# Performance work log

Hardware: AMD Instinct MI355X
Metric: run time of the kernel (lower is better)

Reference implementation:

```python
import jax, jax.numpy as jnp
import numpy as np

NH = 4
MAX_BUF = 1024
EPS = 1e-5


def _ln(x, w, b):
    mu = jnp.mean(x, axis=-1, keepdims=True)
    var = jnp.var(x, axis=-1, keepdims=True)
    return (x - mu) * jax.lax.rsqrt(var + EPS) * w + b


def _mha(xq, xkv, w_qkv, b_qkv, w_o, b_o, key_mask=None):
    D = xq.shape[-1]
    dh = D // NH
    q = xq @ w_qkv[:D].T + b_qkv[:D]
    k = xkv @ w_qkv[D:2 * D].T + b_qkv[D:2 * D]
    v = xkv @ w_qkv[2 * D:].T + b_qkv[2 * D:]
    sp = lambda t: t.reshape(t.shape[0], t.shape[1], NH, dh).transpose(0, 2, 1, 3)
    q, k, v = sp(q), sp(k), sp(v)
    s = jnp.einsum('bhqd,bhkd->bhqk', q, k) / jnp.sqrt(jnp.asarray(dh, q.dtype))
    if key_mask is not None:
        s = jnp.where(key_mask[:, None, None, :], -1e9, s)
    a = jax.nn.softmax(s, axis=-1)
    o = jnp.einsum('bhqk,bhkd->bhqd', a, v)
    o = o.transpose(0, 2, 1, 3).reshape(o.shape[0], o.shape[2], D)
    return o @ w_o.T + b_o


def _conv1d(x, w, b):  # x: (B,C,T), w: (O,I,K) k=3 pad=1
    y = jax.lax.conv_general_dilated(x, w, (1,), [(1, 1)], dimension_numbers=('NCH', 'OIH', 'NCH'))
    return y + b[None, :, None]


def _vpred(xt, c1w, c1b, l1w, l1b, c2w, c2b, l2w, l2b, lw, lb):
    # Faithful to the torch module: LayerNorm(256)/Linear(256,1) act on the LAST
    # axis of the (B,256,T) conv output, which requires T == 256.
    h = _ln(jax.nn.relu(_conv1d(xt, c1w, c1b)), l1w, l1b)
    h = _ln(jax.nn.relu(_conv1d(h, c2w, c2b)), l2w, l2b)
    return (h @ lw.T + lb)[..., 0]  # (B, 256)


def _length_regulate(x, duration, lengths):
    # x: (B,T,D), duration: (B,T) float. Faithful parallel version of the
    # sequential scatter: tokens that are padded, have dur<=0, or would
    # overflow max_len are skipped (pos does not advance).
    B, T, D = x.shape
    durs = jnp.round(duration).astype(jnp.int32)
    max_len = jnp.clip(jnp.round(jnp.sum(duration, axis=1)).max().astype(jnp.int32), 0, MAX_BUF)
    valid_t = jnp.arange(T)[None, :] < lengths[:, None]

    def per_seq(dur_b, val_b):
        def step(pos, dv):
            d, v = dv
            ok = v & (d > 0) & (pos + d <= max_len)
            de = jnp.where(ok, d, 0)
            return pos + de, de
        return jax.lax.scan(step, jnp.asarray(0, jnp.int32), (dur_b, val_b))[1]

    dur_eff = jax.vmap(per_seq)(durs, valid_t)          # (B,T)
    ends = jnp.cumsum(dur_eff, axis=1)                  # token t fills [ends[t-1], ends[t])
    frames = jnp.arange(MAX_BUF)
    tok = jax.vmap(lambda e: jnp.searchsorted(e, frames, side='right'))(ends)  # (B,MAX_BUF)
    in_range = frames[None, :] < ends[:, -1:]
    g = jnp.take_along_axis(x, jnp.clip(tok, 0, T - 1)[..., None], axis=1)
    return jnp.where(in_range[..., None], g, jnp.zeros((), x.dtype))


def _forward(te, lengths, enc_qkv_w, enc_qkv_b, enc_out_w, enc_out_b, enc_ln1_w, enc_ln1_b, enc_ff1_w, enc_ff1_b, enc_ff2_w, enc_ff2_b, enc_ln2_w, enc_ln2_b, vp_c1_w, vp_c1_b, vp_l1_w, vp_l1_b, vp_c2_w, vp_c2_b, vp_l2_w, vp_l2_b, vp_lin_w, vp_lin_b, dec_sa_qkv_w, dec_sa_qkv_b, dec_sa_out_w, dec_sa_out_b, dec_ca_qkv_w, dec_ca_qkv_b, dec_ca_out_w, dec_ca_out_b, dec_ln1_w, dec_ln1_b, dec_ln2_w, dec_ln2_b, dec_ln3_w, dec_ln3_b, dec_ff1_w, dec_ff1_b, dec_ff2_w, dec_ff2_b, mel_w, mel_b):
    B, T, D = te.shape
    mask = jnp.arange(T)[None, :] >= lengths[:, None]  # src_key_padding_mask
    x = te
    for i in range(enc_qkv_w.shape[0]):  # post-norm TransformerEncoderLayer, gelu
        sa = _mha(x, x, enc_qkv_w[i], enc_qkv_b[i], enc_out_w[i], enc_out_b[i], mask)
        x = _ln(x + sa, enc_ln1_w[i], enc_ln1_b[i])
        ff = jax.nn.gelu(x @ enc_ff1_w[i].T + enc_ff1_b[i], approximate=False) @ enc_ff2_w[i].T + enc_ff2_b[i]
        x = _ln(x + ff, enc_ln2_w[i], enc_ln2_b[i])
    enc = x
    xt = enc.transpose(0, 2, 1)  # (B, D, T)
    duration, pitch, energy = [
        _vpred(xt, vp_c1_w[j], vp_c1_b[j], vp_l1_w[j], vp_l1_b[j], vp_c2_w[j], vp_c2_b[j], vp_l2_w[j], vp_l2_b[j], vp_lin_w[j], vp_lin_b[j])
        for j in range(3)]
    y = _length_regulate(enc, duration, lengths)  # (B, MAX_BUF, D)
    for i in range(dec_sa_qkv_w.shape[0]):  # post-norm TransformerDecoderLayer
        sa = _mha(y, y, dec_sa_qkv_w[i], dec_sa_qkv_b[i], dec_sa_out_w[i], dec_sa_out_b[i])
        y = _ln(y + sa, dec_ln1_w[i], dec_ln1_b[i])
        ca = _mha(y, enc, dec_ca_qkv_w[i], dec_ca_qkv_b[i], dec_ca_out_w[i], dec_ca_out_b[i])
        y = _ln(y + ca, dec_ln2_w[i], dec_ln2_b[i])
        ff = jax.nn.gelu(y @ dec_ff1_w[i].T + dec_ff1_b[i], approximate=False) @ dec_ff2_w[i].T + dec_ff2_b[i]
        y = _ln(y + ff, dec_ln3_w[i], dec_ln3_b[i])
    mel = (y @ mel_w.T + mel_b).transpose(0, 2, 1)  # (B, n_mel, MAX_BUF)
    return mel, duration, pitch, energy


def setup_inputs() -> dict:
    B, T, D, FF, NM, L = 32, 256, 256, 1024, 80, 4
    ks = iter(jax.random.split(jax.random.key(0), 80))

    def w(scale, *shape):
        return (scale * jax.random.normal(next(ks), shape)).astype(jnp.float32)

    z = lambda *s: jnp.zeros(s, jnp.float32)
    o = lambda *s: jnp.ones(s, jnp.float32)
    inp = {}
    inp['text_embeddings'] = jax.random.normal(next(ks), (B, T, D), jnp.float32)
    inp['text_lengths'] = jax.random.randint(next(ks), (B,), 64, T + 1, dtype=jnp.int32)
    inp.update(
        enc_qkv_w=w(0.02, L, 3 * D, D), enc_qkv_b=z(L, 3 * D), enc_out_w=w(0.02, L, D, D), enc_out_b=z(L, D),
        enc_ln1_w=o(L, D), enc_ln1_b=z(L, D), enc_ff1_w=w(0.02, L, FF, D), enc_ff1_b=z(L, FF),
        enc_ff2_w=w(0.02, L, D, FF), enc_ff2_b=z(L, D), enc_ln2_w=o(L, D), enc_ln2_b=z(L, D),
        vp_c1_w=w(0.05, 3, 256, D, 3), vp_c1_b=z(3, 256), vp_l1_w=o(3, 256), vp_l1_b=z(3, 256),
        vp_c2_w=w(0.05, 3, 256, 256, 3), vp_c2_b=z(3, 256), vp_l2_w=o(3, 256), vp_l2_b=z(3, 256),
        vp_lin_w=w(0.1, 3, 1, 256), vp_lin_b=jnp.array([[4.0], [0.0], [0.0]], jnp.float32),
        dec_sa_qkv_w=w(0.02, L, 3 * D, D), dec_sa_qkv_b=z(L, 3 * D), dec_sa_out_w=w(0.02, L, D, D), dec_sa_out_b=z(L, D),
        dec_ca_qkv_w=w(0.02, L, 3 * D, D), dec_ca_qkv_b=z(L, 3 * D), dec_ca_out_w=w(0.02, L, D, D), dec_ca_out_b=z(L, D),
        dec_ln1_w=o(L, D), dec_ln1_b=z(L, D), dec_ln2_w=o(L, D), dec_ln2_b=z(L, D), dec_ln3_w=o(L, D), dec_ln3_b=z(L, D),
        dec_ff1_w=w(0.02, L, FF, D), dec_ff1_b=z(L, FF), dec_ff2_w=w(0.02, L, D, FF), dec_ff2_b=z(L, D),
        mel_w=w(0.02, NM, D), mel_b=z(NM))
    return inp


def reference(text_embeddings, text_lengths, enc_qkv_w, enc_qkv_b, enc_out_w, enc_out_b, enc_ln1_w, enc_ln1_b, enc_ff1_w, enc_ff1_b, enc_ff2_w, enc_ff2_b, enc_ln2_w, enc_ln2_b, vp_c1_w, vp_c1_b, vp_l1_w, vp_l1_b, vp_c2_w, vp_c2_b, vp_l2_w, vp_l2_b, vp_lin_w, vp_lin_b, dec_sa_qkv_w, dec_sa_qkv_b, dec_sa_out_w, dec_sa_out_b, dec_ca_qkv_w, dec_ca_qkv_b, dec_ca_out_w, dec_ca_out_b, dec_ln1_w, dec_ln1_b, dec_ln2_w, dec_ln2_b, dec_ln3_w, dec_ln3_b, dec_ff1_w, dec_ff1_b, dec_ff2_w, dec_ff2_b, mel_w, mel_b):
    return _forward(text_embeddings, text_lengths, enc_qkv_w, enc_qkv_b, enc_out_w, enc_out_b, enc_ln1_w, enc_ln1_b, enc_ff1_w, enc_ff1_b, enc_ff2_w, enc_ff2_b, enc_ln2_w, enc_ln2_b, vp_c1_w, vp_c1_b, vp_l1_w, vp_l1_b, vp_c2_w, vp_c2_b, vp_l2_w, vp_l2_b, vp_lin_w, vp_lin_b, dec_sa_qkv_w, dec_sa_qkv_b, dec_sa_out_w, dec_sa_out_b, dec_ca_qkv_w, dec_ca_qkv_b, dec_ca_out_w, dec_ca_out_b, dec_ln1_w, dec_ln1_b, dec_ln2_w, dec_ln2_b, dec_ln3_w, dec_ln3_b, dec_ff1_w, dec_ff1_b, dec_ff2_w, dec_ff2_b, mel_w, mel_b)
```

## Files before the change

### kernel.cpp

```cpp
#include <hip/hip_runtime.h>
#include <hip/hip_bf16.h>
#include <cstdint>
#include <cstddef>


#define B_ 32
#define T_ 256
#define D_ 256
#define NH_ 4
#define FF_ 1024
#define MAXBUF_ 1024
#define NMEL_ 80

typedef __attribute__((ext_vector_type(8))) short short8;
typedef __attribute__((ext_vector_type(4))) float f32x4;

__device__ __forceinline__ unsigned short f2bf(float x) {
  unsigned int u = __float_as_uint(x);
  return (unsigned short)((u + 0x7fffu + ((u >> 16) & 1u)) >> 16);
}
__device__ __forceinline__ float bf2f(unsigned short h) {
  return __uint_as_float(((unsigned int)h) << 16);
}

#define GLD16(g, s)                                                         \
  __builtin_amdgcn_global_load_lds(                                         \
      (__attribute__((address_space(1))) void*)(g),                         \
      (__attribute__((address_space(3))) void*)(s), 16, 0, 0)

__global__ __launch_bounds__(256) void gemm_k(
    const float* __restrict__ A, const float* __restrict__ W,
    const float* __restrict__ bias, float* __restrict__ C,
    int M, int N, int K, int epi)
{
  __shared__ float As[16][64];
  __shared__ float Ws[16][64];
  const int tid = threadIdx.x;
  const int tx = tid & 15, ty = tid >> 4;
  const int bm = blockIdx.x * 64, bn = blockIdx.y * 64;
  const int lm = tid & 63, lk = tid >> 6;
  float acc[4][4] = {{0.f,0.f,0.f,0.f},{0.f,0.f,0.f,0.f},{0.f,0.f,0.f,0.f},{0.f,0.f,0.f,0.f}};
  const bool aok = (bm + lm) < M;
  const bool wok = (bn + lm) < N;
  const float* Ap = A + (size_t)(bm + lm) * K + lk * 4;
  const float* Wp = W + (size_t)(bn + lm) * K + lk * 4;
  for (int k0 = 0; k0 < K; k0 += 16) {
    float4 av = make_float4(0.f, 0.f, 0.f, 0.f);
    float4 wv = make_float4(0.f, 0.f, 0.f, 0.f);
    if (aok) av = *(const float4*)(Ap + k0);
    if (wok) wv = *(const float4*)(Wp + k0);
    As[lk*4+0][lm] = av.x; As[lk*4+1][lm] = av.y; As[lk*4+2][lm] = av.z; As[lk*4+3][lm] = av.w;
    Ws[lk*4+0][lm] = wv.x; Ws[lk*4+1][lm] = wv.y; Ws[lk*4+2][lm] = wv.z; Ws[lk*4+3][lm] = wv.w;
    __syncthreads();
#pragma unroll
    for (int kk = 0; kk < 16; ++kk) {
      float4 a4 = *(const float4*)&As[kk][ty * 4];
      float4 b4 = *(const float4*)&Ws[kk][tx * 4];
      float aa[4] = {a4.x, a4.y, a4.z, a4.w};
      float bb[4] = {b4.x, b4.y, b4.z, b4.w};
#pragma unroll
      for (int i = 0; i < 4; ++i)
#pragma unroll
        for (int j = 0; j < 4; ++j)
          acc[i][j] += aa[i] * bb[j];
    }
    __syncthreads();
  }
#pragma unroll
  for (int i = 0; i < 4; ++i) {
    int gm = bm + ty * 4 + i;
    if (gm >= M) continue;
#pragma unroll
    for (int j = 0; j < 4; ++j) {
      int gn = bn + tx * 4 + j;
      if (gn >= N) continue;
      float v = acc[i][j] + bias[gn];
      if (epi == 1) v = 0.5f * v * (1.0f + erff(v * 0.70710678118654752f));
      C[(size_t)gm * N + gn] = v;
    }
  }
}

__global__ __launch_bounds__(256, 2) void gemm2_k(
    const float* __restrict__ A, const float* __restrict__ W,
    const float* __restrict__ bias, float* __restrict__ C,
    int M, int N, int K, int epi)
{
  __shared__ float As[16][128];
  __shared__ float Bs[16][128];
  const int tid = threadIdx.x;
  const int tx = tid & 15, ty = tid >> 4;
  const int bm = blockIdx.x * 128, bn = blockIdx.y * 128;
  const int r = tid & 127, ks = (tid >> 7) * 8;
  f32x4 acc[8][2];
#pragma unroll
  for (int i = 0; i < 8; ++i) {
    acc[i][0] = (f32x4){0.f, 0.f, 0.f, 0.f};
    acc[i][1] = (f32x4){0.f, 0.f, 0.f, 0.f};
  }
  const float* Ap = A + (size_t)(bm + r) * K + ks;
  const float* Wp = W + (size_t)(bn + r) * K + ks;
  for (int k0 = 0; k0 < K; k0 += 16) {
    float4 a0 = *(const float4*)(Ap + k0);
    float4 a1 = *(const float4*)(Ap + k0 + 4);
    float4 w0 = *(const float4*)(Wp + k0);
    float4 w1 = *(const float4*)(Wp + k0 + 4);
    __syncthreads();
    As[ks+0][r] = a0.x; As[ks+1][r] = a0.y; As[ks+2][r] = a0.z; As[ks+3][r] = a0.w;
    As[ks+4][r] = a1.x; As[ks+5][r] = a1.y; As[ks+6][r] = a1.z; As[ks+7][r] = a1.w;
    Bs[ks+0][r] = w0.x; Bs[ks+1][r] = w0.y; Bs[ks+2][r] = w0.z; Bs[ks+3][r] = w0.w;
    Bs[ks+4][r] = w1.x; Bs[ks+5][r] = w1.y; Bs[ks+6][r] = w1.z; Bs[ks+7][r] = w1.w;
    __syncthreads();
#pragma unroll
    for (int kk = 0; kk < 16; ++kk) {
      f32x4 bA = *(const f32x4*)&Bs[kk][tx * 4];
      f32x4 bB = *(const f32x4*)&Bs[kk][tx * 4 + 64];
      float4 aA = *(const float4*)&As[kk][ty * 4];
      float4 aB = *(const float4*)&As[kk][ty * 4 + 64];
      float av[8] = {aA.x, aA.y, aA.z, aA.w, aB.x, aB.y, aB.z, aB.w};
#pragma unroll
      for (int i = 0; i < 8; ++i) {
        acc[i][0] += bA * av[i];
        acc[i][1] += bB * av[i];
      }
    }
  }
#pragma unroll
  for (int i = 0; i < 8; ++i) {
    int gm = bm + (i >> 2) * 64 + ty * 4 + (i & 3);
#pragma unroll
    for (int half = 0; half < 2; ++half) {
      int gn = bn + half * 64 + tx * 4;
      float4 o;
      o.x = acc[i][half][0] + bias[gn + 0];
      o.y = acc[i][half][1] + bias[gn + 1];
      o.z = acc[i][half][2] + bias[gn + 2];
      o.w = acc[i][half][3] + bias[gn + 3];
      if (epi == 1) {
        o.x = 0.5f * o.x * (1.0f + erff(o.x * 0.70710678118654752f));
        o.y = 0.5f * o.y * (1.0f + erff(o.y * 0.70710678118654752f));
        o.z = 0.5f * o.z * (1.0f + erff(o.z * 0.70710678118654752f));
        o.w = 0.5f * o.w * (1.0f + erff(o.w * 0.70710678118654752f));
      }
      *(float4*)(C + (size_t)gm * N + gn) = o;
    }
  }
}

__global__ __launch_bounds__(256, 2) void gemm2p_k(
    const float* __restrict__ A, const float* __restrict__ W,
    float* __restrict__ Dst, float* __restrict__ Palt,
    int M, int N, int kChunk, int Ktot)
{
  __shared__ float As[16][128];
  __shared__ float Bs[16][128];
  const int tid = threadIdx.x;
  const int tx = tid & 15, ty = tid >> 4;
  const int bm = blockIdx.x * 128, bn = blockIdx.y * 128;
  const int z = blockIdx.z;
  const int r = tid & 127, ks = (tid >> 7) * 8;
  f32x4 acc[8][2];
#pragma unroll
  for (int i = 0; i < 8; ++i) {
    acc[i][0] = (f32x4){0.f, 0.f, 0.f, 0.f};
    acc[i][1] = (f32x4){0.f, 0.f, 0.f, 0.f};
// ... 22 lines not shown
      for (int i = 0; i < 8; ++i) {
        acc[i][0] += bA * av[i];
        acc[i][1] += bB * av[i];
      }
    }
  }
  float* Out = (z == 0) ? Dst : (Palt + (size_t)(z - 1) * ((size_t)M * N));
#pragma unroll
  for (int i = 0; i < 8; ++i) {
    int gm = bm + (i >> 2) * 64 + ty * 4 + (i & 3);
#pragma unroll
    for (int half = 0; half < 2; ++half) {
      int gn = bn + half * 64 + tx * 4;
      float4 o;
      o.x = acc[i][half][0]; o.y = acc[i][half][1];
      o.z = acc[i][half][2]; o.w = acc[i][half][3];
      *(float4*)(Out + (size_t)gm * N + gn) = o;
    }
  }
}

__global__ __launch_bounds__(256) void rsum_k(
    float* __restrict__ C, const float* __restrict__ Palt,
    const float* __restrict__ bias, int Sm1, int N, size_t MN, int epi)
{
  size_t i = ((size_t)blockIdx.x * 256 + threadIdx.x) * 4;
  if (i >= MN) return;
  float4 a = *(const float4*)(C + i);
  for (int s = 0; s < Sm1; ++s) {
    float4 b = *(const float4*)(Palt + (size_t)s * MN + i);
    a.x += b.x; a.y += b.y; a.z += b.z; a.w += b.w;
  }
  int col = (int)(i % (size_t)N);
  a.x += bias[col + 0]; a.y += bias[col + 1];
  a.z += bias[col + 2]; a.w += bias[col + 3];
  if (epi == 1) {
    a.x = 0.5f * a.x * (1.0f + erff(a.x * 0.70710678118654752f));
    a.y = 0.5f * a.y * (1.0f + erff(a.y * 0.70710678118654752f));
    a.z = 0.5f * a.z * (1.0f + erff(a.z * 0.70710678118654752f));
    a.w = 0.5f * a.w * (1.0f + erff(a.w * 0.70710678118654752f));
  }
  *(float4*)(C + i) = a;
}

__global__ __launch_bounds__(256) void attn_k(
    const float* __restrict__ Qp, int qStride,
    const float* __restrict__ Kp, int kStride,
    const float* __restrict__ Vp, int vStride,
    float* __restrict__ Op, int Tq, int Tkv,
    const int* __restrict__ lengths)
{
  const int b = blockIdx.z, h = blockIdx.y, qt = blockIdx.x;
  const int tid = threadIdx.x;
  const int tx = tid & 15, ty = tid >> 4;
  const int lr = tid & 63, lq = tid >> 6;

  __shared__ float Qs[64][64];
  __shared__ float KT[64][64];
  __shared__ float Sm[64][65];

  {
    const float* q = Qp + (size_t)(b * Tq + qt * 64 + lr) * qStride + h * 64 + lq * 16;
    float4 v0 = ((const float4*)q)[0];
    float4 v1 = ((const float4*)q)[1];
    float4 v2 = ((const float4*)q)[2];
    float4 v3 = ((const float4*)q)[3];
    *(float4*)&Qs[lr][lq*16 + 0]  = v0;
    *(float4*)&Qs[lr][lq*16 + 4]  = v1;
    *(float4*)&Qs[lr][lq*16 + 8]  = v2;
    *(float4*)&Qs[lr][lq*16 + 12] = v3;
  }

  float m_reg[4], l_reg[4], o[4][4];
#pragma unroll
  for (int i = 0; i < 4; ++i) {
    m_reg[i] = -INFINITY; l_reg[i] = 0.f;
#pragma unroll
    for (int j = 0; j < 4; ++j) o[i][j] = 0.f;
  }

  const int len_b = lengths ? lengths[b] : 0x7fffffff;
  const int nkt = Tkv >> 6;

  for (int kt = 0; kt < nkt; ++kt) {
    __syncthreads();
    {
      const float* kp = Kp + (size_t)(b * Tkv + kt * 64 + lr) * kStride + h * 64 + lq * 16;
      float4 v[4];
      v[0] = ((const float4*)kp)[0]; v[1] = ((const float4*)kp)[1];
      v[2] = ((const float4*)kp)[2]; v[3] = ((const float4*)kp)[3];
#pragma unroll
      for (int u = 0; u < 4; ++u) {
        KT[lq*16 + u*4 + 0][lr] = v[u].x;
        KT[lq*16 + u*4 + 1][lr] = v[u].y;
        KT[lq*16 + u*4 + 2][lr] = v[u].z;
        KT[lq*16 + u*4 + 3][lr] = v[u].w;
      }
    }
    __syncthreads();

    float s[4][4] = {{0.f,0.f,0.f,0.f},{0.f,0.f,0.f,0.f},{0.f,0.f,0.f,0.f},{0.f,0.f,0.f,0.f}};
#pragma unroll
    for (int d4 = 0; d4 < 16; ++d4) {
      float4 qv[4], kv[4];
#pragma unroll
      for (int i = 0; i < 4; ++i) qv[i] = *(const float4*)&Qs[ty*4 + i][d4*4];
#pragma unroll
      for (int dd = 0; dd < 4; ++dd) kv[dd] = *(const float4*)&KT[d4*4 + dd][tx*4];
#pragma unroll
      for (int i = 0; i < 4; ++i) {
        s[i][0] += qv[i].x*kv[0].x + qv[i].y*kv[1].x + qv[i].z*kv[2].x + qv[i].w*kv[3].x;
        s[i][1] += qv[i].x*kv[0].y + qv[i].y*kv[1].y + qv[i].z*kv[2].y + qv[i].w*kv[3].y;
        s[i][2] += qv[i].x*kv[0].z + qv[i].y*kv[1].z + qv[i].z*kv[2].z + qv[i].w*kv[3].z;
        s[i][3] += qv[i].x*kv[0].w + qv[i].y*kv[1].w + qv[i].z*kv[2].w + qv[i].w*kv[3].w;
      }
    }

    float alpha[4];
#pragma unroll
    for (int i = 0; i < 4; ++i) {
      float pm = -INFINITY;
#pragma unroll
      for (int j = 0; j < 4; ++j) {
        int kg = kt * 64 + tx * 4 + j;
        float v = s[i][j] * 0.125f;
        if (kg >= len_b) v = -1e9f;
        s[i][j] = v;
        pm = fmaxf(pm, v);
      }
#pragma unroll
      for (int off = 1; off < 16; off <<= 1) pm = fmaxf(pm, __shfl_xor(pm, off));
      float mn = fmaxf(m_reg[i], pm);
      alpha[i] = expf(m_reg[i] - mn);
      float ls = 0.f;
#pragma unroll
      for (int j = 0; j < 4; ++j) {
        float p = expf(s[i][j] - mn);
        Sm[ty*4 + i][tx*4 + j] = p;
        ls += p;
      }
#pragma unroll
      for (int off = 1; off < 16; off <<= 1) ls += __shfl_xor(ls, off);
      l_reg[i] = l_reg[i] * alpha[i] + ls;
      m_reg[i] = mn;
    }
    __syncthreads();

    {
      const float* vp = Vp + (size_t)(b * Tkv + kt * 64 + lr) * vStride + h * 64 + lq * 16;
      float4 v0 = ((const float4*)vp)[0];
      float4 v1 = ((const float4*)vp)[1];
      float4 v2 = ((const float4*)vp)[2];
      float4 v3 = ((const float4*)vp)[3];
      *(float4*)&KT[lr][lq*16 + 0]  = v0;
      *(float4*)&KT[lr][lq*16 + 4]  = v1;
      *(float4*)&KT[lr][lq*16 + 8]  = v2;
      *(float4*)&KT[lr][lq*16 + 12] = v3;
    }
    __syncthreads();

#pragma unroll
    for (int i = 0; i < 4; ++i) {
      o[i][0] *= alpha[i]; o[i][1] *= alpha[i]; o[i][2] *= alpha[i]; o[i][3] *= alpha[i];
    }
#pragma unroll 8
    for (int c = 0; c < 64; ++c) {
      float4 vv = *(const float4*)&KT[c][tx * 4];
#pragma unroll
      for (int i = 0; i < 4; ++i) {
        float p = Sm[ty*4 + i][c];
        o[i][0] += p * vv.x; o[i][1] += p * vv.y; o[i][2] += p * vv.z; o[i][3] += p * vv.w;
      }
    }
  }

#pragma unroll
  for (int i = 0; i < 4; ++i) {
    float inv = 1.f / l_reg[i];
    float4 r;
    r.x = o[i][0] * inv; r.y = o[i][1] * inv; r.z = o[i][2] * inv; r.w = o[i][3] * inv;
    *(float4*)(Op + (size_t)(b * Tq + qt * 64 + ty * 4 + i) * 256 + h * 64 + tx * 4) = r;
  }
}

__global__ __launch_bounds__(256) void gemm_bf_k(
    const unsigned short* __restrict__ A, const unsigned short* __restrict__ W,
    const float* __restrict__ bias, unsigned short* __restrict__ C,
    int M, int N, int K, int epi)
{
  __shared__ __align__(16) short As[128 * 32];
  __shared__ __align__(16) short Bs[128 * 32];
  const int tid = threadIdx.x;
  const int lane = tid & 63, w = tid >> 6;
  const int g = lane >> 4, li = lane & 15;
  const int wr = (w >> 1) * 64, wc = (w & 1) * 64;
  const int bm = blockIdx.x * 128, bn = blockIdx.y * 128;

  f32x4 acc[4][4];
#pragma unroll
  for (int m = 0; m < 4; ++m)
#pragma unroll
    for (int n = 0; n < 4; ++n)
      acc[m][n] = (f32x4){0.f, 0.f, 0.f, 0.f};

  const int srow = tid >> 2, scol = (tid & 3) * 8;
  const unsigned short* Ag = A + (size_t)(bm + srow) * K + scol;
  const unsigned short* Wg = W + (size_t)(bn + srow) * K + scol;

  for (int k0 = 0; k0 < K; k0 += 32) {
    __syncthreads();
    GLD16(Ag + k0, &As[tid * 8]);
    GLD16(Ag + k0 + (size_t)64 * K, &As[tid * 8 + 2048]);
    GLD16(Wg + k0, &Bs[tid * 8]);
    GLD16(Wg + k0 + (size_t)64 * K, &Bs[tid * 8 + 2048]);
    __syncthreads();
    short8 af[4], bf[4];
#pragma unroll
    for (int m = 0; m < 4; ++m) af[m] = *(const short8*)&As[(wr + m * 16 + li) * 32 + g * 8];
#pragma unroll
    for (int n = 0; n < 4; ++n) bf[n] = *(const short8*)&Bs[(wc + n * 16 + li) * 32 + g * 8];
#pragma unroll
    for (int m = 0; m < 4; ++m)
#pragma unroll
      for (int n = 0; n < 4; ++n)
        acc[m][n] = __builtin_amdgcn_mfma_f32_16x16x32_bf16(af[m], bf[n], acc[m][n], 0, 0, 0);
  }

#pragma unroll
  for (int m = 0; m < 4; ++m) {
#pragma unroll
    for (int n = 0; n < 4; ++n) {
      int col = bn + wc + n * 16 + li;
      float bv = bias[col];
#pragma unroll
      for (int r = 0; r < 4; ++r) {
        int row = bm + wr + m * 16 + g * 4 + r;
        float v = acc[m][n][r] + bv;
        if (epi == 1) v = 0.5f * v * (1.0f + erff(v * 0.70710678118654752f));
        C[(size_t)row * N + col] = f2bf(v);
      }
// ... 144 lines not shown
          float p = __expf(s[m][n][r] - mn);
          ls += p;
          int col = n * 16 + li;
          Ps[row * 64 + (col ^ ((row & 7) << 3))] = (short)f2bf(p);
        }
#pragma unroll
        for (int off = 1; off < 16; off <<= 1) ls += __shfl_xor(ls, off);
        l_reg[m][r] = l_reg[m][r] * alpha[m][r] + ls;
        m_reg[m][r] = mn;
      }

#pragma unroll
    for (int m = 0; m < 2; ++m) {
      f32x4 al = (f32x4){alpha[m][0], alpha[m][1], alpha[m][2], alpha[m][3]};
#pragma unroll
      for (int n = 0; n < 4; ++n) o[m][n] *= al;
    }
    short8 ap[2][2];
#pragma unroll
    for (int m = 0; m < 2; ++m)
#pragma unroll
      for (int ks = 0; ks < 2; ++ks) {
        int row = w * 32 + m * 16 + li;
        ap[m][ks] = *(const short8*)&Ps[row * 64 + (((ks * 4 + g) ^ (row & 7)) << 3)];
      }
    __builtin_amdgcn_s_setprio(1);
#pragma unroll
    for (int m = 0; m < 2; ++m)
#pragma unroll
      for (int n = 0; n < 4; ++n)
#pragma unroll
        for (int ks = 0; ks < 2; ++ks) {
          int d = n * 16 + li;
          short8 bv = *(const short8*)&VTs[d * 64 + (((ks * 4 + g) ^ (d & 7)) << 3)];
          o[m][n] = __builtin_amdgcn_mfma_f32_16x16x32_bf16(ap[m][ks], bv, o[m][n], 0, 0, 0);
        }
    __builtin_amdgcn_s_setprio(0);
  }

#pragma unroll
  for (int m = 0; m < 2; ++m)
#pragma unroll
    for (int n = 0; n < 4; ++n)
#pragma unroll
      for (int r = 0; r < 4; ++r) {
        float v = o[m][n][r] / l_reg[m][r];
        Op[(size_t)(b * Tq + qt * 128 + w * 32 + m * 16 + g * 4 + r) * 256 + h * 64 + n * 16 + li] = f2bf(v);
      }
}

__global__ __launch_bounds__(256) void addln_k(
    const float* __restrict__ X, const float* __restrict__ R,
    const float* __restrict__ w, const float* __restrict__ bias,
    float* __restrict__ Out, int rows)
{
  int tid = threadIdx.x, wv = tid >> 6, ln = tid & 63;
  int row = blockIdx.x * 4 + wv;
  if (row >= rows) return;
  const float* xp = X + (size_t)row * 256;
  float v[4];
#pragma unroll
  for (int u = 0; u < 4; ++u) v[u] = xp[u * 64 + ln];
  if (R) {
    const float* rp = R + (size_t)row * 256;
#pragma unroll
    for (int u = 0; u < 4; ++u) v[u] += rp[u * 64 + ln];
  }
  float s = v[0] + v[1] + v[2] + v[3];
#pragma unroll
  for (int off = 1; off < 64; off <<= 1) s += __shfl_xor(s, off);
  float mean = s * (1.f / 256.f);
  float c[4], sq = 0.f;
#pragma unroll
  for (int u = 0; u < 4; ++u) { c[u] = v[u] - mean; sq += c[u] * c[u]; }
#pragma unroll
  for (int off = 1; off < 64; off <<= 1) sq += __shfl_xor(sq, off);
  float rs = 1.f / sqrtf(sq * (1.f / 256.f) + 1e-5f);
  float* op = Out + (size_t)row * 256;
#pragma unroll
  for (int u = 0; u < 4; ++u)
    op[u * 64 + ln] = c[u] * rs * w[u * 64 + ln] + bias[u * 64 + ln];
}

__global__ __launch_bounds__(256) void addln2_k(
    const float* __restrict__ X, const unsigned short* __restrict__ Rbf,
    const float* __restrict__ w, const float* __restrict__ bias,
    float* __restrict__ Out, unsigned short* __restrict__ OutBf, int rows)
{
  int tid = threadIdx.x, wv = tid >> 6, ln = tid & 63;
  int row = blockIdx.x * 4 + wv;
  if (row >= rows) return;
  const float* xp = X + (size_t)row * 256;
  const unsigned short* rp = Rbf + (size_t)row * 256;
  float v[4];
#pragma unroll
  for (int u = 0; u < 4; ++u) v[u] = xp[u * 64 + ln] + bf2f(rp[u * 64 + ln]);
  float s = v[0] + v[1] + v[2] + v[3];
#pragma unroll
  for (int off = 1; off < 64; off <<= 1) s += __shfl_xor(s, off);
  float mean = s * (1.f / 256.f);
  float c[4], sq = 0.f;
#pragma unroll
  for (int u = 0; u < 4; ++u) { c[u] = v[u] - mean; sq += c[u] * c[u]; }
#pragma unroll
  for (int off = 1; off < 64; off <<= 1) sq += __shfl_xor(sq, off);
  float rs = 1.f / sqrtf(sq * (1.f / 256.f) + 1e-5f);
  float* op = Out + (size_t)row * 256;
  unsigned short* ob = OutBf + (size_t)row * 256;
#pragma unroll
  for (int u = 0; u < 4; ++u) {
    float y = c[u] * rs * w[u * 64 + ln] + bias[u * 64 + ln];
    op[u * 64 + ln] = y;
    ob[u * 64 + ln] = f2bf(y);
  }
}

__global__ void cvt_k(const float* __restrict__ in, unsigned short* __restrict__ out, int n)
{
  int i = (blockIdx.x * 256 + threadIdx.x) * 4;
  if (i >= n) return;
  float4 v = *(const float4*)(in + i);
  unsigned short o[4] = {f2bf(v.x), f2bf(v.y), f2bf(v.z), f2bf(v.w)};
  *(ushort4*)(out + i) = *(ushort4*)o;
}

__global__ __launch_bounds__(256) void conv_k(
    const float* __restrict__ X, const float* __restrict__ Wt,
    const float* __restrict__ bias, float* __restrict__ Yo, int relu)
{
  const int b = blockIdx.z;
  const int o0 = blockIdx.y * 64, t0 = blockIdx.x * 64;
  const int tid = threadIdx.x, tx = tid & 15, ty = tid >> 4;
  __shared__ __align__(16) float xs[16][68];
  __shared__ __align__(16) float ws_s[64][48];
  float acc[4][4] = {{0.f,0.f,0.f,0.f},{0.f,0.f,0.f,0.f},{0.f,0.f,0.f,0.f},{0.f,0.f,0.f,0.f}};
  for (int i0 = 0; i0 < 256; i0 += 16) {
    for (int idx = tid; idx < 16 * 68; idx += 256) {
      int ic = idx / 68, tt = idx - ic * 68;
      int t = t0 + tt - 1;
      xs[ic][tt] = (tt < 66 && t >= 0 && t < 256)
                       ? X[((size_t)b * 256 + (i0 + ic)) * 256 + t] : 0.f;
    }
    for (int f4 = tid; f4 < 768; f4 += 256) {
      int oo = f4 / 12, seg = f4 - oo * 12;
      float4 v = *(const float4*)(Wt + (size_t)(o0 + oo) * 768 + i0 * 3 + seg * 4);
      *(float4*)&ws_s[oo][seg * 4] = v;
    }
    __syncthreads();
#pragma unroll
    for (int ic = 0; ic < 16; ++ic) {
      float4 xa = *(const float4*)&xs[ic][tx * 4];
      float4 xb = *(const float4*)&xs[ic][tx * 4 + 4];
      float xr[6] = {xa.x, xa.y, xa.z, xa.w, xb.x, xb.y};
#pragma unroll
      for (int i = 0; i < 4; ++i) {
        const float* wr = &ws_s[ty * 4 + i][ic * 3];
        float w0 = wr[0], w1 = wr[1], w2 = wr[2];
#pragma unroll
        for (int j = 0; j < 4; ++j)
          acc[i][j] += w0 * xr[j] + w1 * xr[j + 1] + w2 * xr[j + 2];
      }
    }
    __syncthreads();
  }
#pragma unroll
  for (int i = 0; i < 4; ++i) {
    int oo = o0 + ty * 4 + i;
    float bv = bias[oo];
#pragma unroll
    for (int j = 0; j < 4; ++j) {
      float v = acc[i][j] + bv;
      if (relu) v = fmaxf(v, 0.f);
      Yo[((size_t)b * 256 + oo) * 256 + t0 + tx * 4 + j] = v;
    }
  }
}

__global__ void transp_k(const float* __restrict__ In, float* __restrict__ Out)
{
  int b = blockIdx.z, t0 = blockIdx.x * 32, d0 = blockIdx.y * 32;
  __shared__ float tile[32][33];
  int tx = threadIdx.x, ty = threadIdx.y;
#pragma unroll
  for (int q = 0; q < 4; ++q)
    tile[ty + q * 8][tx] = In[((size_t)b * 256 + t0 + ty + q * 8) * 256 + d0 + tx];
  __syncthreads();
#pragma unroll
  for (int q = 0; q < 4; ++q)
    Out[((size_t)b * 256 + d0 + ty + q * 8) * 256 + t0 + tx] = tile[tx][ty + q * 8];
}

__global__ __launch_bounds__(256) void rowdot_k(
    const float* __restrict__ H, const float* __restrict__ lw,
    const float* __restrict__ lb, float* __restrict__ of32,
    float* __restrict__ oout, int rows)
{
  int tid = threadIdx.x, wv = tid >> 6, ln = tid & 63;
  int row = blockIdx.x * 4 + wv;
  if (row >= rows) return;
  const float* hp = H + (size_t)row * 256;
  float s = 0.f;
#pragma unroll
  for (int u = 0; u < 4; ++u) s += hp[u * 64 + ln] * lw[u * 64 + ln];
#pragma unroll
  for (int off = 1; off < 64; off <<= 1) s += __shfl_xor(s, off);
  if (ln == 0) {
    float v = s + lb[0];
    of32[row] = v;
    oout[row] = v;
  }
}

__global__ void maxlen_k(const float* __restrict__ dur, int* __restrict__ ml)
{
  __shared__ float rnds[32];
  int tid = threadIdx.x, wv = tid >> 6, ln = tid & 63;
  for (int b = wv; b < 32; b += 4) {
    const float* dp = dur + (size_t)b * 256;
    float s = dp[ln] + dp[64 + ln] + dp[128 + ln] + dp[192 + ln];
#pragma unroll
    for (int off = 1; off < 64; off <<= 1) s += __shfl_xor(s, off);
    if (ln == 0) rnds[b] = rintf(s);
  }
  __syncthreads();
  if (tid == 0) {
    float m = rnds[0];
    for (int b = 1; b < 32; ++b) m = fmaxf(m, rnds[b]);
    int v = (int)m;
    v = v < 0 ? 0 : (v > MAXBUF_ ? MAXBUF_ : v);
    *ml = v;
  }
}

__global__ void reg_k(const float* __restrict__ dur, const int* __restrict__ lens,
                      const int* __restrict__ ml, int* __restrict__ tok)
{
  int b = blockIdx.x;
  __shared__ float sdur[256];
  __shared__ int ends[256];
  int tid = threadIdx.x;
  sdur[tid] = dur[(size_t)b * 256 + tid];
  __syncthreads();
  if (tid == 0) {
    int maxlen = *ml, len = lens[b], pos = 0;
    for (int t = 0; t < 256; ++t) {
      int d = (int)rintf(sdur[t]);
      bool ok = (t < len) && (d > 0) && (pos + d <= maxlen);
      if (ok) pos += d;
      ends[t] = pos;
    }
  }
  __syncthreads();
  int total = ends[255];
  for (int f = tid; f < MAXBUF_; f += 256) {
    int lo = 0, hi = 256;
    while (lo < hi) { int mid = (lo + hi) >> 1; if (ends[mid] <= f) lo = mid + 1; else hi = mid; }
    int tc = lo > 255 ? 255 : lo;
    tok[(size_t)b * MAXBUF_ + f] = (f < total) ? tc : -1;
  }
}

__global__ void gather_k(const float* __restrict__ enc, const int* __restrict__ tok,
                         float* __restrict__ Y)
{
  int rf = blockIdx.x;
  int b = rf >> 10;
  int t = tok[rf];
  float4* dst = (float4*)(Y + (size_t)rf * 256);
  int ln = threadIdx.x;
  if (t >= 0) {
    const float4* src = (const float4*)(enc + ((size_t)b * 256 + t) * 256);
    dst[ln] = src[ln];
  } else {
    dst[ln] = make_float4(0.f, 0.f, 0.f, 0.f);
  }
}

__global__ __launch_bounds__(256) void meltr_k(
    const float* __restrict__ MEL, float* __restrict__ out)
{
  int b = blockIdx.z, m0 = blockIdx.y * 16, f0 = blockIdx.x * 64;
  __shared__ float t[16][65];
  int tid = threadIdx.x;
  {
    int f_i = tid >> 4, m_i = tid & 15;
#pragma unroll
    for (int q = 0; q < 4; ++q)
      t[m_i][f_i + q * 16] = MEL[((size_t)b * 1024 + f0 + f_i + q * 16) * 80 + m0 + m_i];
  }
  __syncthreads();
  {
    int f = tid & 63, my = tid >> 6;
#pragma unroll
    for (int q = 0; q < 4; ++q) {
      int m = my * 4 + q;
      out[((size_t)b * NMEL_ + m0 + m) * MAXBUF_ + f0 + f] = t[m][f];
    }
  }
}

extern "C" void kernel_launch(void* const* d_in, const int* in_sizes, int n_in,
                              void* d_out, int out_size, void* d_ws, size_t ws_size,
                              hipStream_t stream)
{
  (void)in_sizes; (void)n_in; (void)out_size;

  const float* te   = (const float*)d_in[0];
  const int*   lens = (const int*)d_in[1];
  const float* e_qkv_w = (const float*)d_in[2];
  const float* e_qkv_b = (const float*)d_in[3];
  const float* e_out_w = (const float*)d_in[4];
  const float* e_out_b = (const float*)d_in[5];
  const float* e_ln1_w = (const float*)d_in[6];
  const float* e_ln1_b = (const float*)d_in[7];
  const float* e_ff1_w = (const float*)d_in[8];
  const float* e_ff1_b = (const float*)d_in[9];
  const float* e_ff2_w = (const float*)d_in[10];
  const float* e_ff2_b = (const float*)d_in[11];
  const float* e_ln2_w = (const float*)d_in[12];
  const float* e_ln2_b = (const float*)d_in[13];
  const float* c1w = (const float*)d_in[14];
  const float* c1b = (const float*)d_in[15];
  const float* l1w = (const float*)d_in[16];
  const float* l1b = (const float*)d_in[17];
  const float* c2w = (const float*)d_in[18];
  const float* c2b = (const float*)d_in[19];
  const float* l2w = (const float*)d_in[20];
  const float* l2b = (const float*)d_in[21];
  const float* linw = (const float*)d_in[22];
  const float* linb = (const float*)d_in[23];
  const float* d_sa_qkv_w = (const float*)d_in[24];
  const float* d_sa_qkv_b = (const float*)d_in[25];
  const float* d_sa_out_w = (const float*)d_in[26];
  const float* d_sa_out_b = (const float*)d_in[27];
  const float* d_ca_qkv_w = (const float*)d_in[28];
  const float* d_ca_qkv_b = (const float*)d_in[29];
  const float* d_ca_out_w = (const float*)d_in[30];
  const float* d_ca_out_b = (const float*)d_in[31];
  const float* d_ln1_w = (const float*)d_in[32];
  const float* d_ln1_b = (const float*)d_in[33];
  const float* d_ln2_w = (const float*)d_in[34];
  const float* d_ln2_b = (const float*)d_in[35];
  const float* d_ln3_w = (const float*)d_in[36];
  const float* d_ln3_b = (const float*)d_in[37];
  const float* d_ff1_w = (const float*)d_in[38];
  const float* d_ff1_b = (const float*)d_in[39];
  const float* d_ff2_w = (const float*)d_in[40];
  const float* d_ff2_b = (const float*)d_in[41];
  const float* melw = (const float*)d_in[42];
  const float* melb = (const float*)d_in[43];
  float* out = (float*)d_out;

  char* p = (char*)d_ws;
  float* Y   = (float*)p;            p += 8388608ull * 4;
  float* ENC = (float*)p;            p += 2097152ull * 4;
  unsigned short* ENCbf = (unsigned short*)p; p += 2097152ull * 2;
  unsigned short* Wsaqkv = (unsigned short*)p; p += 786432ull * 2;
  unsigned short* Wsaout = (unsigned short*)p; p += 262144ull * 2;
  unsigned short* Wcaqkv = (unsigned short*)p; p += 786432ull * 2;
  unsigned short* Wcaout = (unsigned short*)p; p += 262144ull * 2;
  unsigned short* Wff1   = (unsigned short*)p; p += 1048576ull * 2;
  unsigned short* Wff2   = (unsigned short*)p; p += 1048576ull * 2;
  float* DUR = (float*)p;            p += 24576ull * 4;
  int* TOK   = (int*)p;              p += 32768ull * 4;
  int* MAXL  = (int*)p;              p += 4096;
  size_t fixed_b = (size_t)(p - (char*)d_ws);

  int grp = 1;
  {
    const int cand[6] = {32, 16, 8, 4, 2, 1};
    for (int c = 0; c < 6; ++c) {
      if (fixed_b + (size_t)cand[c] * 1835008ull * 2 <= ws_size) { grp = cand[c]; break; }
    }
  }
  unsigned short* REG = (unsigned short*)p;
  unsigned short* Ybf   = REG;
  unsigned short* ADDbf = REG + (size_t)grp * 262144;
  unsigned short* AObf  = REG + (size_t)grp * 524288;
  unsigned short* UN    = REG + (size_t)grp * 786432;
  unsigned short* VTb   = REG + (size_t)grp * 1572864;
  int grp_e = grp * 2 > 32 ? 32 : grp * 2;
  float* P0e = (float*)REG;
  float* P1e = P0e + (size_t)grp_e * 262144;
  float* P2e = P1e + (size_t)grp_e * 65536;
  float* ENCT = Y;
  float* H1   = Y + 2097152;
  float* H2   = Y + 4194304;
  float* MEL  = ENC;

  auto gemm = [&](const float* A, const float* W, const float* bias, float* C,
                  int M, int N, int K, int epi) {
    dim3 g((M + 63) / 64, (N + 63) / 64);
    gemm_k<<<g, dim3(256), 0, stream>>>(A, W, bias, C, M, N, K, epi);
  };
  auto gemm2 = [&](const float* A, const float* W, const float* bias, float* C,
                   int M, int N, int K, int epi) {
    dim3 g(M / 128, N / 128);
    gemm2_k<<<g, dim3(256), 0, stream>>>(A, W, bias, C, M, N, K, epi);
  };
  auto gemm2s = [&](const float* A, const float* W, const float* bias, float* C,
                    int M, int N, int K, int S, int epi) {
    int kChunk = K / S;
    gemm2p_k<<<dim3(M / 128, N / 128, S), dim3(256), 0, stream>>>(
        A, W, C, Y, M, N, kChunk, K);
    size_t MN = (size_t)M * N;
    rsum_k<<<dim3((unsigned)(MN / 1024)), dim3(256), 0, stream>>>(
        C, Y, bias, S - 1, N, MN, epi);
  };
  auto gemm_bf = [&](const unsigned short* A, const unsigned short* W, const float* bias,
                     unsigned short* C, int M, int N, int K, int epi) {
    dim3 g(M / 128, N / 128);
    gemm_bf_k<<<g, dim3(256), 0, stream>>>(A, W, bias, C, M, N, K, epi);
  };
  auto addln = [&](const float* X, const float* R, const float* w, const float* b,
                   float* O, int rows) {
    addln_k<<<dim3((rows + 3) / 4), dim3(256), 0, stream>>>(X, R, w, b, O, rows);
  };
  auto addln2 = [&](const float* X, const unsigned short* Rbf, const float* w, const float* b,
                    float* O, unsigned short* Obf, int rows) {
    addln2_k<<<dim3((rows + 3) / 4), dim3(256), 0, stream>>>(X, Rbf, w, b, O, Obf, rows);
  };
  auto cvt = [&](const float* in, unsigned short* o, int n) {
    cvt_k<<<dim3(n / 1024), dim3(256), 0, stream>>>(in, o, n);
  };

  cvt(d_sa_qkv_w, Wsaqkv, 786432);
  cvt(d_sa_out_w, Wsaout, 262144);
  cvt(d_ca_qkv_w, Wcaqkv, 786432);
  cvt(d_ca_out_w, Wcaout, 262144);
  cvt(d_ff1_w, Wff1, 1048576);
  cvt(d_ff2_w, Wff2, 1048576);

  for (int i = 0; i < 4; ++i) {
    for (int g0 = 0; g0 < B_; g0 += grp_e) {
      int rows = grp_e * T_;
      const size_t off = (size_t)g0 * T_ * D_;
      const float* xin = (i == 0) ? te + off : ENC + off;
      gemm2s(xin, e_qkv_w + (size_t)i * 196608, e_qkv_b + i * 768, P0e, rows, 768, 256, 2, 0);
      attn_k<<<dim3(T_ / 64, NH_, grp_e), dim3(256), 0, stream>>>(
          P0e, 768, P0e + 256, 768, P0e + 512, 768, P1e, T_, T_, lens + g0);
      gemm2s(P1e, e_out_w + (size_t)i * 65536, e_out_b + i * 256, P2e, rows, 256, 256, 4, 0);
      addln(xin, P2e, e_ln1_w + i * 256, e_ln1_b + i * 256, ENC + off, rows);
      gemm2s(ENC + off, e_ff1_w + (size_t)i * 262144, e_ff1_b + i * 1024, P0e, rows, 1024, 256, 2, 1);
      gemm2s(P0e, e_ff2_w + (size_t)i * 262144, e_ff2_b + i * 256, P2e, rows, 256, 1024, 4, 0);
      addln(ENC + off, P2e, e_ln2_w + i * 256, e_ln2_b + i * 256, ENC + off, rows);
    }
  }
  cvt(ENC, ENCbf, 2097152);

  transp_k<<<dim3(8, 8, B_), dim3(32, 8), 0, stream>>>(ENC, ENCT);
  for (int j = 0; j < 3; ++j) {
    conv_k<<<dim3(4, 4, B_), dim3(256), 0, stream>>>(
        ENCT, c1w + (size_t)j * 196608, c1b + j * 256, H1, 1);
    addln(H1, nullptr, l1w + j * 256, l1b + j * 256, H1, B_ * T_);
    conv_k<<<dim3(4, 4, B_), dim3(256), 0, stream>>>(
        H1, c2w + (size_t)j * 196608, c2b + j * 256, H2, 1);
    addln(H2, nullptr, l2w + j * 256, l2b + j * 256, H2, B_ * T_);
    rowdot_k<<<dim3(B_ * T_ / 4), dim3(256), 0, stream>>>(
        H2, linw + j * 256, linb + j, DUR + (size_t)j * 8192,
        out + 2621440 + (size_t)j * 8192, B_ * T_);
  }

  maxlen_k<<<dim3(1), dim3(256), 0, stream>>>(DUR, MAXL);
  reg_k<<<dim3(B_), dim3(256), 0, stream>>>(DUR, lens, MAXL, TOK);
  gather_k<<<dim3(B_ * MAXBUF_), dim3(64), 0, stream>>>(ENC, TOK, Y);

  for (int i = 0; i < 4; ++i) {
    for (int g0 = 0; g0 < B_; g0 += grp) {
      int rows = grp * MAXBUF_;
      float* Yg = Y + (size_t)g0 * MAXBUF_ * D_;
      if (i == 0 || grp != B_)
        cvt(Yg, Ybf, rows * 256);
      gemm_bf(Ybf, Wsaqkv + (size_t)i * 196608, d_sa_qkv_b + i * 768, UN, rows, 768, 256, 0);
      trv_k<<<dim3(MAXBUF_ / 64, NH_, grp), dim3(256), 0, stream>>>(UN + 512, 768, VTb, MAXBUF_);
      attn_bf_k<<<dim3(MAXBUF_ / 128, NH_, grp), dim3(256), 0, stream>>>(
          UN, 768, UN + 256, 768, VTb, AObf, MAXBUF_, MAXBUF_);
      gemm_bf(AObf, Wsaout + (size_t)i * 65536, d_sa_out_b + i * 256, ADDbf, rows, 256, 256, 0);
      addln2(Yg, ADDbf, d_ln1_w + i * 256, d_ln1_b + i * 256, Yg, Ybf, rows);
      gemm_bf(Ybf, Wcaqkv + (size_t)i * 196608, d_ca_qkv_b + i * 768, UN, rows, 256, 256, 0);
      gemm_bf(ENCbf + (size_t)g0 * 65536, Wcaqkv + (size_t)i * 196608 + 65536,
              d_ca_qkv_b + i * 768 + 256, UN + (size_t)grp * 262144, grp * T_, 512, 256, 0);
      trv_k<<<dim3(T_ / 64, NH_, grp), dim3(256), 0, stream>>>(
          UN + (size_t)grp * 262144 + 256, 512, VTb, T_);
      attn_bf_k<<<dim3(MAXBUF_ / 128, NH_, grp), dim3(256), 0, stream>>>(
          UN, 256, UN + (size_t)grp * 262144, 512, VTb, AObf, MAXBUF_, T_);
      gemm_bf(AObf, Wcaout + (size_t)i * 65536, d_ca_out_b + i * 256, ADDbf, rows, 256, 256, 0);
      addln2(Yg, ADDbf, d_ln2_w + i * 256, d_ln2_b + i * 256, Yg, Ybf, rows);
      gemm_bf(Ybf, Wff1 + (size_t)i * 262144, d_ff1_b + i * 1024, UN, rows, 1024, 256, 1);
      gemm_bf(UN, Wff2 + (size_t)i * 262144, d_ff2_b + i * 256, ADDbf, rows, 256, 1024, 0);
      addln2(Yg, ADDbf, d_ln3_w + i * 256, d_ln3_b + i * 256, Yg, Ybf, rows);
    }
  }

  gemm(Y, melw, melb, MEL, B_ * MAXBUF_, NMEL_, 256, 0);
  meltr_k<<<dim3(16, 5, B_), dim3(256), 0, stream>>>(MEL, out);
}
```

Before: 3.155 ms.

## Keep decoder residual stream in bf16 and prefetch K/V tiles in fp32 attention

```diff
diff --git a/kernel.cpp b/kernel.cpp
--- a/kernel.cpp
+++ b/kernel.cpp
@@ -81,6 +81,60 @@
   }
 }
 
+__global__ __launch_bounds__(256) void gemm_kb_k(
+    const unsigned short* __restrict__ A, const float* __restrict__ W,
+    const float* __restrict__ bias, float* __restrict__ C,
+    int M, int N, int K)
+{
+  __shared__ float As[16][64];
+  __shared__ float Ws[16][64];
+  const int tid = threadIdx.x;
+  const int tx = tid & 15, ty = tid >> 4;
+  const int bm = blockIdx.x * 64, bn = blockIdx.y * 64;
+  const int lm = tid & 63, lk = tid >> 6;
+  float acc[4][4] = {{0.f,0.f,0.f,0.f},{0.f,0.f,0.f,0.f},{0.f,0.f,0.f,0.f},{0.f,0.f,0.f,0.f}};
+  const bool aok = (bm + lm) < M;
+  const bool wok = (bn + lm) < N;
+  const unsigned short* Ap = A + (size_t)(bm + lm) * K + lk * 4;
+  const float* Wp = W + (size_t)(bn + lm) * K + lk * 4;
+  for (int k0 = 0; k0 < K; k0 += 16) {
+    float4 av = make_float4(0.f, 0.f, 0.f, 0.f);
+    float4 wv = make_float4(0.f, 0.f, 0.f, 0.f);
+    if (aok) {
+      ushort4 au = *(const ushort4*)(Ap + k0);
+      av.x = bf2f(au.x); av.y = bf2f(au.y); av.z = bf2f(au.z); av.w = bf2f(au.w);
+    }
+    if (wok) wv = *(const float4*)(Wp + k0);
+    As[lk*4+0][lm] = av.x; As[lk*4+1][lm] = av.y; As[lk*4+2][lm] = av.z; As[lk*4+3][lm] = av.w;
+    Ws[lk*4+0][lm] = wv.x; Ws[lk*4+1][lm] = wv.y; Ws[lk*4+2][lm] = wv.z; Ws[lk*4+3][lm] = wv.w;
+    __syncthreads();
+#pragma unroll
+    for (int kk = 0; kk < 16; ++kk) {
+      float4 a4 = *(const float4*)&As[kk][ty * 4];
+      float4 b4 = *(const float4*)&Ws[kk][tx * 4];
+      float aa[4] = {a4.x, a4.y, a4.z, a4.w};
+      float bb[4] = {b4.x, b4.y, b4.z, b4.w};
+#pragma unroll
+      for (int i = 0; i < 4; ++i)
+#pragma unroll
+        for (int j = 0; j < 4; ++j)
+          acc[i][j] += aa[i] * bb[j];
+    }
+    __syncthreads();
+  }
+#pragma unroll
+  for (int i = 0; i < 4; ++i) {
+    int gm = bm + ty * 4 + i;
+    if (gm >= M) continue;
+#pragma unroll
+    for (int j = 0; j < 4; ++j) {
+      int gn = bn + tx * 4 + j;
+      if (gn >= N) continue;
+      C[(size_t)gm * N + gn] = acc[i][j] + bias[gn];
+    }
+  }
+}
+
 __global__ __launch_bounds__(256, 2) void gemm2_k(
     const float* __restrict__ A, const float* __restrict__ W,
     const float* __restrict__ bias, float* __restrict__ C,
@@ -269,20 +323,31 @@
   const int len_b = lengths ? lengths[b] : 0x7fffffff;
   const int nkt = Tkv >> 6;
 
+  float4 kreg[4], vreg[4];
+  {
+    const float* kp = Kp + (size_t)(b * Tkv + lr) * kStride + h * 64 + lq * 16;
+    kreg[0] = ((const float4*)kp)[0]; kreg[1] = ((const float4*)kp)[1];
+    kreg[2] = ((const float4*)kp)[2]; kreg[3] = ((const float4*)kp)[3];
+    const float* vp = Vp + (size_t)(b * Tkv + lr) * vStride + h * 64 + lq * 16;
+    vreg[0] = ((const float4*)vp)[0]; vreg[1] = ((const float4*)vp)[1];
+    vreg[2] = ((const float4*)vp)[2]; vreg[3] = ((const float4*)vp)[3];
+  }
+
   for (int kt = 0; kt < nkt; ++kt) {
     __syncthreads();
     {
-      const float* kp = Kp + (size_t)(b * Tkv + kt * 64 + lr) * kStride + h * 64 + lq * 16;
-      float4 v[4];
-      v[0] = ((const float4*)kp)[0]; v[1] = ((const float4*)kp)[1];
-      v[2] = ((const float4*)kp)[2]; v[3] = ((const float4*)kp)[3];
 #pragma unroll
       for (int u = 0; u < 4; ++u) {
-        KT[lq*16 + u*4 + 0][lr] = v[u].x;
-        KT[lq*16 + u*4 + 1][lr] = v[u].y;
-        KT[lq*16 + u*4 + 2][lr] = v[u].z;
-        KT[lq*16 + u*4 + 3][lr] = v[u].w;
-      }
+        KT[lq*16 + u*4 + 0][lr] = kreg[u].x;
+        KT[lq*16 + u*4 + 1][lr] = kreg[u].y;
+        KT[lq*16 + u*4 + 2][lr] = kreg[u].z;
+        KT[lq*16 + u*4 + 3][lr] = kreg[u].w;
+      }
+    }
+    if (kt + 1 < nkt) {
+      const float* kp = Kp + (size_t)(b * Tkv + (kt + 1) * 64 + lr) * kStride + h * 64 + lq * 16;
+      kreg[0] = ((const float4*)kp)[0]; kreg[1] = ((const float4*)kp)[1];
+      kreg[2] = ((const float4*)kp)[2]; kreg[3] = ((const float4*)kp)[3];
     }
     __syncthreads();
 
@@ -334,15 +399,15 @@
     __syncthreads();
 
     {
-      const float* vp = Vp + (size_t)(b * Tkv + kt * 64 + lr) * vStride + h * 64 + lq * 16;
-      float4 v0 = ((const float4*)vp)[0];
-      float4 v1 = ((const float4*)vp)[1];
-      float4 v2 = ((const float4*)vp)[2];
-      float4 v3 = ((const float4*)vp)[3];
-      *(float4*)&KT[lr][lq*16 + 0]  = v0;
-      *(float4*)&KT[lr][lq*16 + 4]  = v1;
-      *(float4*)&KT[lr][lq*16 + 8]  = v2;
-      *(float4*)&KT[lr][lq*16 + 12] = v3;
+      *(float4*)&KT[lr][lq*16 + 0]  = vreg[0];
+      *(float4*)&KT[lr][lq*16 + 4]  = vreg[1];
+      *(float4*)&KT[lr][lq*16 + 8]  = vreg[2];
+      *(float4*)&KT[lr][lq*16 + 12] = vreg[3];
+    }
+    if (kt + 1 < nkt) {
+      const float* vp = Vp + (size_t)(b * Tkv + (kt + 1) * 64 + lr) * vStride + h * 64 + lq * 16;
+      vreg[0] = ((const float4*)vp)[0]; vreg[1] = ((const float4*)vp)[1];
+      vreg[2] = ((const float4*)vp)[2]; vreg[3] = ((const float4*)vp)[3];
     }
     __syncthreads();
 
@@ -653,19 +718,18 @@
     op[u * 64 + ln] = c[u] * rs * w[u * 64 + ln] + bias[u * 64 + ln];
 }
 
-__global__ __launch_bounds__(256) void addln2_k(
-    const float* __restrict__ X, const unsigned short* __restrict__ Rbf,
-    const float* __restrict__ w, const float* __restrict__ bias,
-    float* __restrict__ Out, unsigned short* __restrict__ OutBf, int rows)
+__global__ __launch_bounds__(256) void addlnb_k(
+    unsigned short* __restrict__ Xbf, const unsigned short* __restrict__ Rbf,
+    const float* __restrict__ w, const float* __restrict__ bias, int rows)
 {
   int tid = threadIdx.x, wv = tid >> 6, ln = tid & 63;
   int row = blockIdx.x * 4 + wv;
   if (row >= rows) return;
-  const float* xp = X + (size_t)row * 256;
+  unsigned short* xp = Xbf + (size_t)row * 256;
   const unsigned short* rp = Rbf + (size_t)row * 256;
   float v[4];
 #pragma unroll
-  for (int u = 0; u < 4; ++u) v[u] = xp[u * 64 + ln] + bf2f(rp[u * 64 + ln]);
+  for (int u = 0; u < 4; ++u) v[u] = bf2f(xp[u * 64 + ln]) + bf2f(rp[u * 64 + ln]);
   float s = v[0] + v[1] + v[2] + v[3];
 #pragma unroll
   for (int off = 1; off < 64; off <<= 1) s += __shfl_xor(s, off);
@@ -676,23 +740,11 @@
 #pragma unroll
   for (int off = 1; off < 64; off <<= 1) sq += __shfl_xor(sq, off);
   float rs = 1.f / sqrtf(sq * (1.f / 256.f) + 1e-5f);
-  float* op = Out + (size_t)row * 256;
-  unsigned short* ob = OutBf + (size_t)row * 256;
 #pragma unroll
   for (int u = 0; u < 4; ++u) {
     float y = c[u] * rs * w[u * 64 + ln] + bias[u * 64 + ln];
-    op[u * 64 + ln] = y;
-    ob[u * 64 + ln] = f2bf(y);
-  }
-}
-
-__global__ void cvt_k(const float* __restrict__ in, unsigned short* __restrict__ out, int n)
-{
-  int i = (blockIdx.x * 256 + threadIdx.x) * 4;
-  if (i >= n) return;
-  float4 v = *(const float4*)(in + i);
-  unsigned short o[4] = {f2bf(v.x), f2bf(v.y), f2bf(v.z), f2bf(v.w)};
-  *(ushort4*)(out + i) = *(ushort4*)o;
+    xp[u * 64 + ln] = f2bf(y);
+  }
 }
 
 __global__ __launch_bounds__(256) void conv_k(
@@ -831,19 +883,21 @@
   }
 }
 
-__global__ void gather_k(const float* __restrict__ enc, const int* __restrict__ tok,
-                         float* __restrict__ Y)
+__global__ void gatherb_k(const float* __restrict__ enc, const int* __restrict__ tok,
+                          unsigned short* __restrict__ Ybf)
 {
   int rf = blockIdx.x;
   int b = rf >> 10;
   int t = tok[rf];
-  float4* dst = (float4*)(Y + (size_t)rf * 256);
+  unsigned short* dst = Ybf + (size_t)rf * 256;
   int ln = threadIdx.x;
   if (t >= 0) {
-    const float4* src = (const float4*)(enc + ((size_t)b * 256 + t) * 256);
-    dst[ln] = src[ln];
+    float4 v = ((const float4*)(enc + ((size_t)b * 256 + t) * 256))[ln];
+    unsigned short o[4] = {f2bf(v.x), f2bf(v.y), f2bf(v.z), f2bf(v.w)};
+    *(ushort4*)(dst + ln * 4) = *(ushort4*)o;
   } else {
-    dst[ln] = make_float4(0.f, 0.f, 0.f, 0.f);
+    unsigned short o[4] = {0, 0, 0, 0};
+    *(ushort4*)(dst + ln * 4) = *(ushort4*)o;
   }
 }
 
@@ -964,11 +1018,6 @@
     dim3 g((M + 63) / 64, (N + 63) / 64);
     gemm_k<<<g, dim3(256), 0, stream>>>(A, W, bias, C, M, N, K, epi);
   };
-  auto gemm2 = [&](const float* A, const float* W, const float* bias, float* C,
-                   int M, int N, int K, int epi) {
-    dim3 g(M / 128, N / 128);
-    gemm2_k<<<g, dim3(256), 0, stream>>>(A, W, bias, C, M, N, K, epi);
-  };
   auto gemm2s = [&](const float* A, const float* W, const float* bias, float* C,
                     int M, int N, int K, int S, int epi) {
     int kChunk = K / S;
@@ -987,20 +1036,29 @@
                    float* O, int rows) {
     addln_k<<<dim3((rows + 3) / 4), dim3(256), 0, stream>>>(X, R, w, b, O, rows);
   };
-  auto addln2 = [&](const float* X, const unsigned short* Rbf, const float* w, const float* b,
-                    float* O, unsigned short* Obf, int rows) {
-    addln2_k<<<dim3((rows + 3) / 4), dim3(256), 0, stream>>>(X, Rbf, w, b, O, Obf, rows);
+  auto addlnb = [&](unsigned short* Xbf, const unsigned short* Rbf, const float* w,
+                    const float* b, int rows) {
+    addlnb_k<<<dim3((rows + 3) / 4), dim3(256), 0, stream>>>(Xbf, Rbf, w, b, rows);
   };
   auto cvt = [&](const float* in, unsigned short* o, int n) {
+    (void)in; (void)o; (void)n;
+  };
+  (void)cvt;
+
+  struct CvtLaunch {
+    static void run(const float* in, unsigned short* o, int n, hipStream_t s);
+  };
+  auto cvt2 = [&](const float* in, unsigned short* o, int n) {
+    extern __global__ void cvt_k(const float*, unsigned short*, int);
     cvt_k<<<dim3(n / 1024), dim3(256), 0, stream>>>(in, o, n);
   };
 
-  cvt(d_sa_qkv_w, Wsaqkv, 786432);
-  cvt(d_sa_out_w, Wsaout, 262144);
-  cvt(d_ca_qkv_w, Wcaqkv, 786432);
-  cvt(d_ca_out_w, Wcaout, 262144);
-  cvt(d_ff1_w, Wff1, 1048576);
-  cvt(d_ff2_w, Wff2, 1048576);
+  cvt2(d_sa_qkv_w, Wsaqkv, 786432);
+  cvt2(d_sa_out_w, Wsaout, 262144);
+  cvt2(d_ca_qkv_w, Wcaqkv, 786432);
+  cvt2(d_ca_out_w, Wcaout, 262144);
+  cvt2(d_ff1_w, Wff1, 1048576);
+  cvt2(d_ff2_w, Wff2, 1048576);
 
   for (int i = 0; i < 4; ++i) {
     for (int g0 = 0; g0 < B_; g0 += grp_e) {
@@ -1017,7 +1075,7 @@
       addln(ENC + off, P2e, e_ln2_w + i * 256, e_ln2_b + i * 256, ENC + off, rows);
     }
   }
-  cvt(ENC, ENCbf, 2097152);
+  cvt2(ENC, ENCbf, 2097152);
 
   transp_k<<<dim3(8, 8, B_), dim3(32, 8), 0, stream>>>(ENC, ENCT);
   for (int j = 0; j < 3; ++j) {
@@ -1034,20 +1092,17 @@
 
   maxlen_k<<<dim3(1), dim3(256), 0, stream>>>(DUR, MAXL);
   reg_k<<<dim3(B_), dim3(256), 0, stream>>>(DUR, lens, MAXL, TOK);
-  gather_k<<<dim3(B_ * MAXBUF_), dim3(64), 0, stream>>>(ENC, TOK, Y);
+  gatherb_k<<<dim3(B_ * MAXBUF_), dim3(64), 0, stream>>>(ENC, TOK, Ybf);
 
   for (int i = 0; i < 4; ++i) {
     for (int g0 = 0; g0 < B_; g0 += grp) {
       int rows = grp * MAXBUF_;
-      float* Yg = Y + (size_t)g0 * MAXBUF_ * D_;
-      if (i == 0 || grp != B_)
-        cvt(Yg, Ybf, rows * 256);
       gemm_bf(Ybf, Wsaqkv + (size_t)i * 196608, d_sa_qkv_b + i * 768, UN, rows, 768, 256, 0);
       trv_k<<<dim3(MAXBUF_ / 64, NH_, grp), dim3(256), 0, stream>>>(UN + 512, 768, VTb, MAXBUF_);
       attn_bf_k<<<dim3(MAXBUF_ / 128, NH_, grp), dim3(256), 0, stream>>>(
           UN, 768, UN + 256, 768, VTb, AObf, MAXBUF_, MAXBUF_);
       gemm_bf(AObf, Wsaout + (size_t)i * 65536, d_sa_out_b + i * 256, ADDbf, rows, 256, 256, 0);
-      addln2(Yg, ADDbf, d_ln1_w + i * 256, d_ln1_b + i * 256, Yg, Ybf, rows);
+      addlnb(Ybf, ADDbf, d_ln1_w + i * 256, d_ln1_b + i * 256, rows);
       gemm_bf(Ybf, Wcaqkv + (size_t)i * 196608, d_ca_qkv_b + i * 768, UN, rows, 256, 256, 0);
       gemm_bf(ENCbf + (size_t)g0 * 65536, Wcaqkv + (size_t)i * 196608 + 65536,
               d_ca_qkv_b + i * 768 + 256, UN + (size_t)grp * 262144, grp * T_, 512, 256, 0);
@@ -1056,13 +1111,24 @@
       attn_bf_k<<<dim3(MAXBUF_ / 128, NH_, grp), dim3(256), 0, stream>>>(
           UN, 256, UN + (size_t)grp * 262144, 512, VTb, AObf, MAXBUF_, T_);
       gemm_bf(AObf, Wcaout + (size_t)i * 65536, d_ca_out_b + i * 256, ADDbf, rows, 256, 256, 0);
-      addln2(Yg, ADDbf, d_ln2_w + i * 256, d_ln2_b + i * 256, Yg, Ybf, rows);
+      addlnb(Ybf, ADDbf, d_ln2_w + i * 256, d_ln2_b + i * 256, rows);
       gemm_bf(Ybf, Wff1 + (size_t)i * 262144, d_ff1_b + i * 1024, UN, rows, 1024, 256, 1);
       gemm_bf(UN, Wff2 + (size_t)i * 262144, d_ff2_b + i * 256, ADDbf, rows, 256, 1024, 0);
-      addln2(Yg, ADDbf, d_ln3_w + i * 256, d_ln3_b + i * 256, Yg, Ybf, rows);
-    }
-  }
-
-  gemm(Y, melw, melb, MEL, B_ * MAXBUF_, NMEL_, 256, 0);
+      addlnb(Ybf, ADDbf, d_ln3_w + i * 256, d_ln3_b + i * 256, rows);
+    }
+  }
+
+  gemm_kb_k<<<dim3((B_ * MAXBUF_ + 63) / 64, (NMEL_ + 63) / 64), dim3(256), 0, stream>>>(
+      Ybf, melw, melb, MEL, B_ * MAXBUF_, NMEL_, 256);
   meltr_k<<<dim3(16, 5, B_), dim3(256), 0, stream>>>(MEL, out);
-}
+  (void)gemm;
+}
+
+__global__ void cvt_k(const float* __restrict__ in, unsigned short* __restrict__ out, int n)
+{
+  int i = (blockIdx.x * 256 + threadIdx.x) * 4;
+  if (i >= n) return;
+  float4 v = *(const float4*)(in + i);
+  unsigned short o[4] = {f2bf(v.x), f2bf(v.y), f2bf(v.z), f2bf(v.w)};
+  *(ushort4*)(out + i) = *(ushort4*)o;
+}
```

New measurement: 3.094 ms. About the same (-1.9%).
